# Kernel tuning notes

Hardware: AMD Instinct MI355X
Metric: run time of the kernel (lower is better)

Reference implementation:

```python
import jax, jax.numpy as jnp
import numpy as np

B, S, D, P, NQ = 8, 2048, 1024, 256, 8192


def setup_inputs() -> dict:
    key = jax.random.key(0)
    ks = jax.random.split(key, 8)
    return {
        "flag": 0,
        "encoded_input": jax.random.normal(ks[0], (B, S, D), dtype=jnp.float32),
        "start_ids_1": jax.random.randint(ks[1], (NQ,), 0, S, dtype=jnp.int32),
        "end_ids_1": jax.random.randint(ks[2], (NQ,), 0, S, dtype=jnp.int32),
        "query_batch_idx": jax.random.randint(ks[3], (NQ,), 0, B, dtype=jnp.int32),
        "start_ids_2": jax.random.randint(ks[4], (NQ,), 0, S, dtype=jnp.int32),
        "end_ids_2": jax.random.randint(ks[5], (NQ,), 0, S, dtype=jnp.int32),
        "W": jax.random.normal(ks[6], (D, P), dtype=jnp.float32) * 0.02,
        "b": jnp.zeros((P,), dtype=jnp.float32),
    }


def _gather_spans(h, qb, s, e):
    # span_repr[b, i, j] = concat(h[b, i], h[b, j]) for j >= i, else 0.
    # Direct gather instead of building the O(seq^2) table.
    rep = jnp.concatenate([h[qb, s], h[qb, e]], axis=-1)  # [NQ, 2*P]
    valid = (e >= s).astype(rep.dtype)[:, None]
    return rep * valid


def reference(flag, encoded_input, start_ids_1, end_ids_1, query_batch_idx,
              start_ids_2, end_ids_2, W, b):
    h = encoded_input @ W + b  # [B, S, P] (use_proj=True)
    res1 = _gather_spans(h, query_batch_idx, start_ids_1, end_ids_1)
    res2 = _gather_spans(h, query_batch_idx, start_ids_2, end_ids_2)
    return (res1, res2)
```

## Files before the change

kernel.cpp:

```cpp
#include <hip/hip_runtime.h>
#include <hip/hip_bf16.h>
#include <stdint.h>

#define S_LEN 2048
#define D_DIM 1024
#define P_DIM 256
#define NQ_   8192
#define M_TOT 16384
#define CAP 32
#define HS  260

typedef __attribute__((ext_vector_type(4))) float  f32x4;
typedef __attribute__((ext_vector_type(8))) __bf16 bf16x8;


__global__ __launch_bounds__(1024) void wtf_kernel(const float* __restrict__ W,
                                                   __bf16* __restrict__ WTf,
                                                   int* __restrict__ cnt) {
    __shared__ float tile[32][33];
    const int bx = blockIdx.x;
    const int by = blockIdx.y;
    const int k0 = bx * 32, n0 = by * 32;
    const int tx = threadIdx.x, ty = threadIdx.y;
    const int g = (by * 32 + bx) * 1024 + ty * 32 + tx;
    if (g < M_TOT) cnt[g] = 0;
    tile[ty][tx] = W[(k0 + ty) * P_DIM + (n0 + tx)];
    __syncthreads();
    const int t = ty * 32 + tx;
    if (t < 128) {
        const int c16r = t >> 6, q = (t >> 4) & 3, lm = t & 15;
        bf16x8 v;
        #pragma unroll
        for (int e = 0; e < 8; ++e) v[e] = (__bf16)tile[q * 8 + e][c16r * 16 + lm];
        const int c16 = by * 2 + c16r;
        const int ts  = bx >> 1, kh = bx & 1;
        *(bf16x8*)(WTf + (size_t)((c16 * 32 + ts * 2 + kh) * 512 + (q * 16 + lm) * 8)) = v;
    }
}

__global__ __launch_bounds__(256) void index_zero(const int* __restrict__ s1,
                                                  const int* __restrict__ e1,
                                                  const int* __restrict__ s2,
                                                  const int* __restrict__ e2,
                                                  const int* __restrict__ qb,
                                                  int* __restrict__ cnt,
                                                  int* __restrict__ bucket,
                                                  float* __restrict__ out) {
    const int lane = threadIdx.x & 63;
    const int q    = blockIdx.x * 64 + lane;
    const int set  = threadIdx.x >> 7;
    const int half = (threadIdx.x >> 6) & 1;
    const int b    = qb[q];
    const int s = set ? s2[q] : s1[q];
    const int e = set ? e2[q] : e1[q];
    if (!half && e >= s) {
        int r = b * S_LEN + s;
        int k = atomicAdd(&cnt[r], 1); if (k < CAP) bucket[r * CAP + k] = (q << 2) | (set << 1);
        r = b * S_LEN + e;
        k = atomicAdd(&cnt[r], 1);     if (k < CAP) bucket[r * CAP + k] = (q << 2) | (set << 1) | 1;
    }
    unsigned long long mask = __ballot(e < s);
    const int bqw = blockIdx.x * 64;
    const float4 z = make_float4(0.f, 0.f, 0.f, 0.f);
    while (mask) {
        const int j = __ffsll(mask) - 1;
        mask &= mask - 1;
        float* dst = out + (size_t)set * (NQ_ * 512) + (size_t)(bqw + j) * 512 + half * 256;
        ((float4*)dst)[lane] = z;
    }
}

__global__ __launch_bounds__(512, 1) void gemm_kernel(const float*  __restrict__ A,
                                                      const __bf16* __restrict__ WTf,
                                                      const float*  __restrict__ bias,
                                                      const int*    __restrict__ cnt,
                                                      const int*    __restrict__ bucket,
                                                      float*        __restrict__ out) {
    __shared__ __align__(16) __bf16 Afl[65536];
    __shared__ int s_cnt[64];
    __shared__ int s_off[65];
    __shared__ int elist[64 * CAP];

    const int tid = threadIdx.x;
    const int w   = tid >> 6;
    const int l   = tid & 63;
    const int lm  = l & 15;
    const int q   = l >> 4;

    const int m0  = blockIdx.x * 64;
    const int ph4 = blockIdx.x & 3;

    const __bf16* bp[2][2];
    #pragma unroll
    for (int ni = 0; ni < 2; ++ni)
        #pragma unroll
        for (int kh = 0; kh < 2; ++kh)
            bp[ni][kh] = WTf + (size_t)(((w * 2 + ni) * 32 + kh) * 512 + l * 8);

    bf16x8 bre[3][2][2];
#define KT_OF(T) ((((ph4 + ((T) >> 2)) & 3) << 2) + ((T) & 3))
#define LOADB(B, T) {                                                         \
    const int kt_ = KT_OF(T);                                                 \
    _Pragma("unroll") for (int ni = 0; ni < 2; ++ni)                          \
        _Pragma("unroll") for (int kh = 0; kh < 2; ++kh)                      \
            bre[B][ni][kh] = *(const bf16x8*)(bp[ni][kh] + kt_ * 1024); }

    LOADB(0, 0)
    LOADB(1, 1)

    const int r    = tid >> 3;
    const int la   = tid & 7;
    const int mi_s = r >> 4, lmr = r & 15;
    const float* asrc = A + (size_t)(m0 + r) * D_DIM;

    float4 fA[8], fB[8];
#define LOADQ(QQ, FR) {                                                       \
    _Pragma("unroll") for (int it = 0; it < 4; ++it) {                        \
        const int c = (QQ) * 32 + it * 8 + la;                                \
        FR[it * 2]     = *(const float4*)(asrc + c * 8);                      \
        FR[it * 2 + 1] = *(const float4*)(asrc + c * 8 + 4); } }
#define WRITEQ(QQ, FR) {                                                      \
    _Pragma("unroll") for (int it = 0; it < 4; ++it) {                        \
        const int c = (QQ) * 32 + it * 8 + la;                                \
        bf16x8 v;                                                             \
        v[0] = (__bf16)FR[it*2].x;   v[1] = (__bf16)FR[it*2].y;               \
        v[2] = (__bf16)FR[it*2].z;   v[3] = (__bf16)FR[it*2].w;               \
        v[4] = (__bf16)FR[it*2+1].x; v[5] = (__bf16)FR[it*2+1].y;             \
        v[6] = (__bf16)FR[it*2+1].z; v[7] = (__bf16)FR[it*2+1].w;             \
        const int kt = c >> 3, kh = (c >> 2) & 1, qp = c & 3;                 \
        const int slot = lmr ^ (qp << 1);                                     \
        *(bf16x8*)(&Afl[(mi_s * 32 + kt * 2 + kh) * 512 + qp * 128 + slot * 8]) = v; } }

    const int slotr = lm ^ (q << 1);
    const __bf16* abase = Afl + q * 128 + slotr * 8;
    f32x4 acc[4][2] = {};

#define CSTEP(T) {                                                            \
    const int kt_ = KT_OF(T);                                                 \
    bf16x8 af[4][2];                                                          \
    _Pragma("unroll") for (int mi = 0; mi < 4; ++mi)                          \
        _Pragma("unroll") for (int kh = 0; kh < 2; ++kh)                      \
            af[mi][kh] = *(const bf16x8*)(abase + (mi * 32 + kt_ * 2 + kh) * 512); \
    _Pragma("unroll") for (int kh = 0; kh < 2; ++kh)                          \
        _Pragma("unroll") for (int mi = 0; mi < 4; ++mi)                      \
            _Pragma("unroll") for (int ni = 0; ni < 2; ++ni)                  \
                acc[mi][ni] = __builtin_amdgcn_mfma_f32_16x16x32_bf16(        \
                    af[mi][kh], bre[(T) % 3][ni][kh], acc[mi][ni], 0, 0, 0); }

    const int q0 = ph4, q1 = (ph4 + 1) & 3, q2 = (ph4 + 2) & 3, q3 = (ph4 + 3) & 3;

    LOADQ(q0, fA)
    LOADQ(q1, fB)
    WRITEQ(q0, fA)
    __syncthreads();
    LOADB(2, 2) CSTEP(0) LOADB(0, 3) CSTEP(1) LOADB(1, 4) CSTEP(2) LOADB(2, 5) CSTEP(3)
    WRITEQ(q1, fB)
    LOADQ(q2, fA)
    __syncthreads();
    LOADB(0, 6) CSTEP(4) LOADB(1, 7) CSTEP(5) LOADB(2, 8) CSTEP(6) LOADB(0, 9) CSTEP(7)
    WRITEQ(q2, fA)
    LOADQ(q3, fB)
    __syncthreads();
    LOADB(1, 10) CSTEP(8) LOADB(2, 11) CSTEP(9) LOADB(0, 12) CSTEP(10) LOADB(1, 13) CSTEP(11)
    WRITEQ(q3, fB)
    __syncthreads();
    LOADB(2, 14) CSTEP(12) LOADB(0, 15) CSTEP(13) CSTEP(14) CSTEP(15)

#undef CSTEP
#undef LOADQ
#undef WRITEQ
#undef LOADB
#undef KT_OF

    __syncthreads();
    float* hs = (float*)Afl;

    if (tid < 64) { int c = cnt[m0 + tid]; s_cnt[tid] = c < CAP ? c : CAP; }

    #pragma unroll
    for (int ni = 0; ni < 2; ++ni) {
        const int col = w * 32 + ni * 16 + lm;
        const float bv = bias[col];
        #pragma unroll
        for (int mi = 0; mi < 4; ++mi) {
            const int rbase = mi * 16 + q * 4;
            #pragma unroll
            for (int rr = 0; rr < 4; ++rr)
                hs[(rbase + rr) * HS + col] = acc[mi][ni][rr] + bv;
        }
    }
    __syncthreads();
    if (tid == 0) {
        int a = 0;
        #pragma unroll 1
        for (int i = 0; i < 64; ++i) { s_off[i] = a; a += s_cnt[i]; }
        s_off[64] = a;
    }
    __syncthreads();
    if (tid < 64) {
        const int o = s_off[tid], c = s_cnt[tid];
        const int* bk = bucket + (size_t)(m0 + tid) * CAP;
        for (int k = 0; k < c; ++k)
            elist[o + k] = (tid << 15) | (bk[k] & 0x7fff);
    }
    __syncthreads();

    const int E   = s_off[64];
    const int grp = tid >> 6;
    const int gl  = tid & 63;
    #pragma unroll 1
    for (int j = grp; j < E; j += 8) {
        const int ent  = elist[j];
        const int rl   = ent >> 15;
        const int code = ent & 0x7fff;
        const int qq   = code >> 2;
        const int st   = (code >> 1) & 1;
        const int hf   = code & 1;
        const float4 v = *(const float4*)&hs[rl * HS + gl * 4];
        *(float4*)(out + (size_t)st * (NQ_ * 512) + (size_t)qq * 512 + hf * 256 + gl * 4) = v;
    }
}

extern "C" void kernel_launch(void* const* d_in, const int* in_sizes, int n_in,
                              void* d_out, int out_size, void* d_ws, size_t ws_size,
                              hipStream_t stream) {
    const float* A    = (const float*)d_in[1];
    const int*   s1   = (const int*)  d_in[2];
    const int*   e1   = (const int*)  d_in[3];
    const int*   qb   = (const int*)  d_in[4];
    const int*   s2   = (const int*)  d_in[5];
    const int*   e2   = (const int*)  d_in[6];
    const float* W    = (const float*)d_in[7];
    const float* bias = (const float*)d_in[8];
    float*       out  = (float*)d_out;

    __bf16* WTf    = (__bf16*)d_ws;
    int*    cnt    = (int*)((char*)d_ws + (1 << 20));
    int*    bucket = (int*)((char*)d_ws + (1 << 20) + (1 << 16));

    wtf_kernel <<<dim3(32, 8), dim3(32, 32), 0, stream>>>(W, WTf, cnt);
    index_zero <<<dim3(NQ_ / 64), dim3(256), 0, stream>>>(s1, e1, s2, e2, qb, cnt, bucket, out);
    gemm_kernel<<<dim3(M_TOT / 64), dim3(512), 0, stream>>>(A, WTf, bias, cnt, bucket, out);
}
```

Measured before the change: 132.5 us.

## Fuse weight prep, indexing and GEMM into one cooperative kernel with grid syncs

Merges the three launches (W transpose/convert, span bucketing plus zeroing, GEMM with scatter) into a single cooperative kernel of 256 blocks. Two grid-wide barriers order the phases: W conversion and count reset first, then bucket atomics, then the GEMM. A-tile loads are issued before the barriers so global latency overlaps the prep work. This removes kernel launch gaps and inter-kernel drains, at the cost of grid-sync overhead and needing all 256 blocks co-resident at one block per CU.

Result: slower. 215.7 us (+62.7%).

```diff
diff --git a/kernel.cpp b/kernel.cpp
--- a/kernel.cpp
+++ b/kernel.cpp
@@ -1,6 +1,9 @@
 #include <hip/hip_runtime.h>
+#include <hip/hip_cooperative_groups.h>
 #include <hip/hip_bf16.h>
 #include <stdint.h>
+
+namespace cg = cooperative_groups;
 
 #define S_LEN 2048
 #define D_DIM 1024
@@ -14,68 +17,18 @@
 typedef __attribute__((ext_vector_type(8))) __bf16 bf16x8;
 
 
-__global__ __launch_bounds__(1024) void wtf_kernel(const float* __restrict__ W,
-                                                   __bf16* __restrict__ WTf,
-                                                   int* __restrict__ cnt) {
-    __shared__ float tile[32][33];
-    const int bx = blockIdx.x;
-    const int by = blockIdx.y;
-    const int k0 = bx * 32, n0 = by * 32;
-    const int tx = threadIdx.x, ty = threadIdx.y;
-    const int g = (by * 32 + bx) * 1024 + ty * 32 + tx;
-    if (g < M_TOT) cnt[g] = 0;
-    tile[ty][tx] = W[(k0 + ty) * P_DIM + (n0 + tx)];
-    __syncthreads();
-    const int t = ty * 32 + tx;
-    if (t < 128) {
-        const int c16r = t >> 6, q = (t >> 4) & 3, lm = t & 15;
-        bf16x8 v;
-        #pragma unroll
-        for (int e = 0; e < 8; ++e) v[e] = (__bf16)tile[q * 8 + e][c16r * 16 + lm];
-        const int c16 = by * 2 + c16r;
-        const int ts  = bx >> 1, kh = bx & 1;
-        *(bf16x8*)(WTf + (size_t)((c16 * 32 + ts * 2 + kh) * 512 + (q * 16 + lm) * 8)) = v;
-    }
-}
-
-__global__ __launch_bounds__(256) void index_zero(const int* __restrict__ s1,
-                                                  const int* __restrict__ e1,
-                                                  const int* __restrict__ s2,
-                                                  const int* __restrict__ e2,
-                                                  const int* __restrict__ qb,
-                                                  int* __restrict__ cnt,
-                                                  int* __restrict__ bucket,
-                                                  float* __restrict__ out) {
-    const int lane = threadIdx.x & 63;
-    const int q    = blockIdx.x * 64 + lane;
-    const int set  = threadIdx.x >> 7;
-    const int half = (threadIdx.x >> 6) & 1;
-    const int b    = qb[q];
-    const int s = set ? s2[q] : s1[q];
-    const int e = set ? e2[q] : e1[q];
-    if (!half && e >= s) {
-        int r = b * S_LEN + s;
-        int k = atomicAdd(&cnt[r], 1); if (k < CAP) bucket[r * CAP + k] = (q << 2) | (set << 1);
-        r = b * S_LEN + e;
-        k = atomicAdd(&cnt[r], 1);     if (k < CAP) bucket[r * CAP + k] = (q << 2) | (set << 1) | 1;
-    }
-    unsigned long long mask = __ballot(e < s);
-    const int bqw = blockIdx.x * 64;
-    const float4 z = make_float4(0.f, 0.f, 0.f, 0.f);
-    while (mask) {
-        const int j = __ffsll(mask) - 1;
-        mask &= mask - 1;
-        float* dst = out + (size_t)set * (NQ_ * 512) + (size_t)(bqw + j) * 512 + half * 256;
-        ((float4*)dst)[lane] = z;
-    }
-}
-
-__global__ __launch_bounds__(512, 1) void gemm_kernel(const float*  __restrict__ A,
-                                                      const __bf16* __restrict__ WTf,
-                                                      const float*  __restrict__ bias,
-                                                      const int*    __restrict__ cnt,
-                                                      const int*    __restrict__ bucket,
-                                                      float*        __restrict__ out) {
+__global__ __launch_bounds__(512, 1) void fused_kernel(const float*  __restrict__ A,
+                                                       const float*  __restrict__ W,
+                                                       const float*  __restrict__ bias,
+                                                       const int*    __restrict__ s1,
+                                                       const int*    __restrict__ e1,
+                                                       const int*    __restrict__ s2,
+                                                       const int*    __restrict__ e2,
+                                                       const int*    __restrict__ qb,
+                                                       int*          __restrict__ cnt,
+                                                       int*          __restrict__ bucket,
+                                                       __bf16*       __restrict__ WTf,
+                                                       float*        __restrict__ out) {
     __shared__ __align__(16) __bf16 Afl[65536];
     __shared__ int s_cnt[64];
     __shared__ int s_off[65];
@@ -87,26 +40,9 @@
     const int lm  = l & 15;
     const int q   = l >> 4;
 
-    const int m0  = blockIdx.x * 64;
-    const int ph4 = blockIdx.x & 3;
-
-    const __bf16* bp[2][2];
-    #pragma unroll
-    for (int ni = 0; ni < 2; ++ni)
-        #pragma unroll
-        for (int kh = 0; kh < 2; ++kh)
-            bp[ni][kh] = WTf + (size_t)(((w * 2 + ni) * 32 + kh) * 512 + l * 8);
-
-    bf16x8 bre[3][2][2];
-#define KT_OF(T) ((((ph4 + ((T) >> 2)) & 3) << 2) + ((T) & 3))
-#define LOADB(B, T) {                                                         \
-    const int kt_ = KT_OF(T);                                                 \
-    _Pragma("unroll") for (int ni = 0; ni < 2; ++ni)                          \
-        _Pragma("unroll") for (int kh = 0; kh < 2; ++kh)                      \
-            bre[B][ni][kh] = *(const bf16x8*)(bp[ni][kh] + kt_ * 1024); }
-
-    LOADB(0, 0)
-    LOADB(1, 1)
+    const int bx  = blockIdx.x;
+    const int m0  = bx * 64;
+    const int ph4 = bx & 3;
 
     const int r    = tid >> 3;
     const int la   = tid & 7;
@@ -131,6 +67,81 @@
         const int slot = lmr ^ (qp << 1);                                     \
         *(bf16x8*)(&Afl[(mi_s * 32 + kt * 2 + kh) * 512 + qp * 128 + slot * 8]) = v; } }
 
+    const int q0 = ph4, q1 = (ph4 + 1) & 3, q2 = (ph4 + 2) & 3, q3 = (ph4 + 3) & 3;
+
+    LOADQ(q0, fA)
+    LOADQ(q1, fB)
+
+    if (tid < 64) cnt[bx * 64 + tid] = 0;
+
+    {
+        float* wscr = (float*)elist;
+        const int kx = bx & 31, ny = bx >> 5;
+        const int tx = tid & 31, ty0 = tid >> 5;
+        wscr[ty0 * 33 + tx]        = W[(kx * 32 + ty0) * P_DIM + ny * 32 + tx];
+        wscr[(ty0 + 16) * 33 + tx] = W[(kx * 32 + ty0 + 16) * P_DIM + ny * 32 + tx];
+        __syncthreads();
+        if (tid < 128) {
+            const int c16r = tid >> 6, qq = (tid >> 4) & 3, lmm = tid & 15;
+            bf16x8 v;
+            #pragma unroll
+            for (int e = 0; e < 8; ++e) v[e] = (__bf16)wscr[(qq * 8 + e) * 33 + c16r * 16 + lmm];
+            const int c16 = ny * 2 + c16r, ts = kx >> 1, kh = kx & 1;
+            *(bf16x8*)(WTf + (size_t)((c16 * 32 + ts * 2 + kh) * 512 + (qq * 16 + lmm) * 8)) = v;
+        }
+    }
+
+    WRITEQ(q0, fA)
+
+    const int gw = bx * 8 + w;
+    int sv = 0, ev = -1, bv = 0, seth = 0, halfh = 0, qz = 0, bqw = 0;
+    if (gw < 512) {
+        seth  = (gw >> 1) & 1;
+        halfh = gw & 1;
+        bqw   = (gw >> 2) * 64;
+        qz    = bqw + l;
+        bv    = qb[qz];
+        sv    = seth ? s2[qz] : s1[qz];
+        ev    = seth ? e2[qz] : e1[qz];
+        unsigned long long mask = __ballot(ev < sv);
+        const float4 z = make_float4(0.f, 0.f, 0.f, 0.f);
+        while (mask) {
+            const int j = __ffsll(mask) - 1;
+            mask &= mask - 1;
+            float* dst = out + (size_t)seth * (NQ_ * 512) + (size_t)(bqw + j) * 512 + halfh * 256;
+            ((float4*)dst)[l] = z;
+        }
+    }
+
+    cg::this_grid().sync();
+
+    const __bf16* bp[2][2];
+    #pragma unroll
+    for (int ni = 0; ni < 2; ++ni)
+        #pragma unroll
+        for (int kh = 0; kh < 2; ++kh)
+            bp[ni][kh] = WTf + (size_t)(((w * 2 + ni) * 32 + kh) * 512 + l * 8);
+
+    bf16x8 bre[3][2][2];
+#define KT_OF(T) ((((ph4 + ((T) >> 2)) & 3) << 2) + ((T) & 3))
+#define LOADB(B, T) {                                                         \
+    const int kt_ = KT_OF(T);                                                 \
+    _Pragma("unroll") for (int ni = 0; ni < 2; ++ni)                          \
+        _Pragma("unroll") for (int kh = 0; kh < 2; ++kh)                      \
+            bre[B][ni][kh] = *(const bf16x8*)(bp[ni][kh] + kt_ * 1024); }
+
+    LOADB(0, 0)
+    LOADB(1, 1)
+
+    if (gw < 512 && !halfh && ev >= sv) {
+        int rr = bv * S_LEN + sv;
+        int k = atomicAdd(&cnt[rr], 1); if (k < CAP) bucket[rr * CAP + k] = (qz << 2) | (seth << 1);
+        rr = bv * S_LEN + ev;
+        k = atomicAdd(&cnt[rr], 1);     if (k < CAP) bucket[rr * CAP + k] = (qz << 2) | (seth << 1) | 1;
+    }
+
+    cg::this_grid().sync();
+
     const int slotr = lm ^ (q << 1);
     const __bf16* abase = Afl + q * 128 + slotr * 8;
     f32x4 acc[4][2] = {};
@@ -147,12 +158,6 @@
                 acc[mi][ni] = __builtin_amdgcn_mfma_f32_16x16x32_bf16(        \
                     af[mi][kh], bre[(T) % 3][ni][kh], acc[mi][ni], 0, 0, 0); }
 
-    const int q0 = ph4, q1 = (ph4 + 1) & 3, q2 = (ph4 + 2) & 3, q3 = (ph4 + 3) & 3;
-
-    LOADQ(q0, fA)
-    LOADQ(q1, fB)
-    WRITEQ(q0, fA)
-    __syncthreads();
     LOADB(2, 2) CSTEP(0) LOADB(0, 3) CSTEP(1) LOADB(1, 4) CSTEP(2) LOADB(2, 5) CSTEP(3)
     WRITEQ(q1, fB)
     LOADQ(q2, fA)
@@ -180,13 +185,13 @@
     #pragma unroll
     for (int ni = 0; ni < 2; ++ni) {
         const int col = w * 32 + ni * 16 + lm;
-        const float bv = bias[col];
+        const float bv2 = bias[col];
         #pragma unroll
         for (int mi = 0; mi < 4; ++mi) {
             const int rbase = mi * 16 + q * 4;
             #pragma unroll
             for (int rr = 0; rr < 4; ++rr)
-                hs[(rbase + rr) * HS + col] = acc[mi][ni][rr] + bv;
+                hs[(rbase + rr) * HS + col] = acc[mi][ni][rr] + bv2;
         }
     }
     __syncthreads();
@@ -205,11 +210,10 @@
     }
     __syncthreads();
 
-    const int E   = s_off[64];
-    const int grp = tid >> 6;
-    const int gl  = tid & 63;
+    const int E  = s_off[64];
+    const int gl = l;
     #pragma unroll 1
-    for (int j = grp; j < E; j += 8) {
+    for (int j = w; j < E; j += 8) {
         const int ent  = elist[j];
         const int rl   = ent >> 15;
         const int code = ent & 0x7fff;
@@ -238,7 +242,9 @@
     int*    cnt    = (int*)((char*)d_ws + (1 << 20));
     int*    bucket = (int*)((char*)d_ws + (1 << 20) + (1 << 16));
 
-    wtf_kernel <<<dim3(32, 8), dim3(32, 32), 0, stream>>>(W, WTf, cnt);
-    index_zero <<<dim3(NQ_ / 64), dim3(256), 0, stream>>>(s1, e1, s2, e2, qb, cnt, bucket, out);
-    gemm_kernel<<<dim3(M_TOT / 64), dim3(512), 0, stream>>>(A, WTf, bias, cnt, bucket, out);
+    void* args[] = { (void*)&A, (void*)&W, (void*)&bias,
+                     (void*)&s1, (void*)&e1, (void*)&s2, (void*)&e2, (void*)&qb,
+                     (void*)&cnt, (void*)&bucket, (void*)&WTf, (void*)&out };
+    hipLaunchCooperativeKernel((void*)fused_kernel, dim3(M_TOT / 64), dim3(512),
+                               args, 0, stream);
 }
```

## Fuse span indexing into GEMM kernel with per-block query scans

Applied to the files above, without the earlier changes.

Removes the separate index_zero kernel and its global cnt/bucket tables. Each GEMM block now scans all queries in both sets, picks the ones whose start or end row falls in its 64-row tile, and builds per-wave entry lists in shared memory while the first A loads are in flight. Zeroing of invalid spans also moves into the GEMM kernel. This saves a kernel launch and the global atomics. In exchange every block redundantly reads all 16K index pairs, and each wave's list is capped at 256 entries.

Result: slower. 140.7 us (+6.2%).

```diff
diff --git a/kernel.cpp b/kernel.cpp
--- a/kernel.cpp
+++ b/kernel.cpp
@@ -7,23 +7,20 @@
 #define P_DIM 256
 #define NQ_   8192
 #define M_TOT 16384
-#define CAP 32
 #define HS  260
+#define WCAP 256
 
 typedef __attribute__((ext_vector_type(4))) float  f32x4;
 typedef __attribute__((ext_vector_type(8))) __bf16 bf16x8;
 
 
 __global__ __launch_bounds__(1024) void wtf_kernel(const float* __restrict__ W,
-                                                   __bf16* __restrict__ WTf,
-                                                   int* __restrict__ cnt) {
+                                                   __bf16* __restrict__ WTf) {
     __shared__ float tile[32][33];
     const int bx = blockIdx.x;
     const int by = blockIdx.y;
     const int k0 = bx * 32, n0 = by * 32;
     const int tx = threadIdx.x, ty = threadIdx.y;
-    const int g = (by * 32 + bx) * 1024 + ty * 32 + tx;
-    if (g < M_TOT) cnt[g] = 0;
     tile[ty][tx] = W[(k0 + ty) * P_DIM + (n0 + tx)];
     __syncthreads();
     const int t = ty * 32 + tx;
@@ -38,48 +35,18 @@
     }
 }
 
-__global__ __launch_bounds__(256) void index_zero(const int* __restrict__ s1,
-                                                  const int* __restrict__ e1,
-                                                  const int* __restrict__ s2,
-                                                  const int* __restrict__ e2,
-                                                  const int* __restrict__ qb,
-                                                  int* __restrict__ cnt,
-                                                  int* __restrict__ bucket,
-                                                  float* __restrict__ out) {
-    const int lane = threadIdx.x & 63;
-    const int q    = blockIdx.x * 64 + lane;
-    const int set  = threadIdx.x >> 7;
-    const int half = (threadIdx.x >> 6) & 1;
-    const int b    = qb[q];
-    const int s = set ? s2[q] : s1[q];
-    const int e = set ? e2[q] : e1[q];
-    if (!half && e >= s) {
-        int r = b * S_LEN + s;
-        int k = atomicAdd(&cnt[r], 1); if (k < CAP) bucket[r * CAP + k] = (q << 2) | (set << 1);
-        r = b * S_LEN + e;
-        k = atomicAdd(&cnt[r], 1);     if (k < CAP) bucket[r * CAP + k] = (q << 2) | (set << 1) | 1;
-    }
-    unsigned long long mask = __ballot(e < s);
-    const int bqw = blockIdx.x * 64;
-    const float4 z = make_float4(0.f, 0.f, 0.f, 0.f);
-    while (mask) {
-        const int j = __ffsll(mask) - 1;
-        mask &= mask - 1;
-        float* dst = out + (size_t)set * (NQ_ * 512) + (size_t)(bqw + j) * 512 + half * 256;
-        ((float4*)dst)[lane] = z;
-    }
-}
-
 __global__ __launch_bounds__(512, 1) void gemm_kernel(const float*  __restrict__ A,
                                                       const __bf16* __restrict__ WTf,
                                                       const float*  __restrict__ bias,
-                                                      const int*    __restrict__ cnt,
-                                                      const int*    __restrict__ bucket,
+                                                      const int*    __restrict__ s1,
+                                                      const int*    __restrict__ e1,
+                                                      const int*    __restrict__ s2,
+                                                      const int*    __restrict__ e2,
+                                                      const int*    __restrict__ qb,
                                                       float*        __restrict__ out) {
     __shared__ __align__(16) __bf16 Afl[65536];
-    __shared__ int s_cnt[64];
-    __shared__ int s_off[65];
-    __shared__ int elist[64 * CAP];
+    __shared__ int elist[8 * WCAP];
+    __shared__ int sEw[8];
 
     const int tid = threadIdx.x;
     const int w   = tid >> 6;
@@ -87,8 +54,11 @@
     const int lm  = l & 15;
     const int q   = l >> 4;
 
-    const int m0  = blockIdx.x * 64;
-    const int ph4 = blockIdx.x & 3;
+    const int bx  = blockIdx.x;
+    const int m0  = bx * 64;
+    const int ph4 = bx & 3;
+
+    if (l == 0) sEw[w] = 0;
 
     const __bf16* bp[2][2];
     #pragma unroll
@@ -131,6 +101,55 @@
         const int slot = lmr ^ (qp << 1);                                     \
         *(bf16x8*)(&Afl[(mi_s * 32 + kt * 2 + kh) * 512 + qp * 128 + slot * 8]) = v; } }
 
+    const int q0 = ph4, q1 = (ph4 + 1) & 3, q2 = (ph4 + 2) & 3, q3 = (ph4 + 3) & 3;
+
+    LOADQ(q0, fA)
+    LOADQ(q1, fB)
+
+    #pragma unroll
+    for (int set = 0; set < 2; ++set) {
+        const int* sA = set ? s2 : s1;
+        const int* eA = set ? e2 : e1;
+        #pragma unroll 4
+        for (int i = 0; i < 16; ++i) {
+            const int qq = w * 1024 + i * 64 + l;
+            const int s  = sA[qq];
+            const int e  = eA[qq];
+            if (e >= s) {
+                const int b  = qb[qq];
+                const int rs = b * S_LEN + s - m0;
+                const int re = b * S_LEN + e - m0;
+                if ((unsigned)rs < 64u) {
+                    const int k = atomicAdd(&sEw[w], 1);
+                    if (k < WCAP) elist[w * WCAP + k] = (rs << 15) | (qq << 2) | (set << 1);
+                }
+                if ((unsigned)re < 64u) {
+                    const int k = atomicAdd(&sEw[w], 1);
+                    if (k < WCAP) elist[w * WCAP + k] = (re << 15) | (qq << 2) | (set << 1) | 1;
+                }
+            }
+        }
+    }
+    {
+        const float4 z = make_float4(0.f, 0.f, 0.f, 0.f);
+        #pragma unroll 1
+        for (int p = 0; p < 8; ++p) {
+            const int pair = w * 8 + p;
+            const int qq   = bx * 32 + (pair >> 1);
+            const int set  = pair & 1;
+            const int s = set ? s2[qq] : s1[qq];
+            const int e = set ? e2[qq] : e1[qq];
+            if (e < s) {
+                float* dst = out + (size_t)set * (NQ_ * 512) + (size_t)qq * 512;
+                ((float4*)dst)[l]      = z;
+                ((float4*)dst)[l + 64] = z;
+            }
+        }
+    }
+
+    WRITEQ(q0, fA)
+    __syncthreads();
+
     const int slotr = lm ^ (q << 1);
     const __bf16* abase = Afl + q * 128 + slotr * 8;
     f32x4 acc[4][2] = {};
@@ -147,12 +166,6 @@
                 acc[mi][ni] = __builtin_amdgcn_mfma_f32_16x16x32_bf16(        \
                     af[mi][kh], bre[(T) % 3][ni][kh], acc[mi][ni], 0, 0, 0); }
 
-    const int q0 = ph4, q1 = (ph4 + 1) & 3, q2 = (ph4 + 2) & 3, q3 = (ph4 + 3) & 3;
-
-    LOADQ(q0, fA)
-    LOADQ(q1, fB)
-    WRITEQ(q0, fA)
-    __syncthreads();
     LOADB(2, 2) CSTEP(0) LOADB(0, 3) CSTEP(1) LOADB(1, 4) CSTEP(2) LOADB(2, 5) CSTEP(3)
     WRITEQ(q1, fB)
     LOADQ(q2, fA)
@@ -174,8 +187,6 @@
 
     __syncthreads();
     float* hs = (float*)Afl;
-
-    if (tid < 64) { int c = cnt[m0 + tid]; s_cnt[tid] = c < CAP ? c : CAP; }
 
     #pragma unroll
     for (int ni = 0; ni < 2; ++ni) {
@@ -190,34 +201,18 @@
         }
     }
     __syncthreads();
-    if (tid == 0) {
-        int a = 0;
-        #pragma unroll 1
-        for (int i = 0; i < 64; ++i) { s_off[i] = a; a += s_cnt[i]; }
-        s_off[64] = a;
-    }
-    __syncthreads();
-    if (tid < 64) {
-        const int o = s_off[tid], c = s_cnt[tid];
-        const int* bk = bucket + (size_t)(m0 + tid) * CAP;
-        for (int k = 0; k < c; ++k)
-            elist[o + k] = (tid << 15) | (bk[k] & 0x7fff);
-    }
-    __syncthreads();
-
-    const int E   = s_off[64];
-    const int grp = tid >> 6;
-    const int gl  = tid & 63;
+
+    const int E = sEw[w] < WCAP ? sEw[w] : WCAP;
     #pragma unroll 1
-    for (int j = grp; j < E; j += 8) {
-        const int ent  = elist[j];
+    for (int j = 0; j < E; ++j) {
+        const int ent  = elist[w * WCAP + j];
         const int rl   = ent >> 15;
         const int code = ent & 0x7fff;
         const int qq   = code >> 2;
         const int st   = (code >> 1) & 1;
         const int hf   = code & 1;
-        const float4 v = *(const float4*)&hs[rl * HS + gl * 4];
-        *(float4*)(out + (size_t)st * (NQ_ * 512) + (size_t)qq * 512 + hf * 256 + gl * 4) = v;
+        const float4 v = *(const float4*)&hs[rl * HS + l * 4];
+        *(float4*)(out + (size_t)st * (NQ_ * 512) + (size_t)qq * 512 + hf * 256 + l * 4) = v;
     }
 }
 
@@ -234,11 +229,9 @@
     const float* bias = (const float*)d_in[8];
     float*       out  = (float*)d_out;
 
-    __bf16* WTf    = (__bf16*)d_ws;
-    int*    cnt    = (int*)((char*)d_ws + (1 << 20));
-    int*    bucket = (int*)((char*)d_ws + (1 << 20) + (1 << 16));
-
-    wtf_kernel <<<dim3(32, 8), dim3(32, 32), 0, stream>>>(W, WTf, cnt);
-    index_zero <<<dim3(NQ_ / 64), dim3(256), 0, stream>>>(s1, e1, s2, e2, qb, cnt, bucket, out);
-    gemm_kernel<<<dim3(M_TOT / 64), dim3(512), 0, stream>>>(A, WTf, bias, cnt, bucket, out);
+    __bf16* WTf = (__bf16*)d_ws;
+
+    wtf_kernel <<<dim3(32, 8), dim3(32, 32), 0, stream>>>(W, WTf);
+    gemm_kernel<<<dim3(M_TOT / 64), dim3(512), 0, stream>>>(A, WTf, bias,
+                                                            s1, e1, s2, e2, qb, out);
 }
```
